# Performance work log

Hardware: AMD Instinct MI355X
Metric: run time of the kernel (lower is better)

The kernel has to match this reference:

```python
import jax, jax.numpy as jnp
import numpy as np

EMB = 300
NUM_LAYERS = 5
ATOM_DIMS = [119, 4, 12, 12, 10, 6, 6, 2, 2]
BOND_DIMS = [5, 6, 2]
BN_EPS = 1e-5


def setup_inputs() -> dict:
    key = jax.random.key(0)
    ks = jax.random.split(key, 16)
    N, E = 100000, 200000
    x_feat = jax.random.randint(ks[0], (N, 9), 0, 2, dtype=jnp.int32)
    edge_index = jax.random.randint(ks[1], (2, E), 0, N, dtype=jnp.int32)
    edge_attr = jax.random.randint(ks[2], (E, 3), 0, 2, dtype=jnp.int32)
    # atom embedding tables padded to max atom dim 119: [9, 119, EMB]
    atom_emb = jax.random.normal(ks[3], (9, max(ATOM_DIMS), EMB), jnp.float32) * 0.1
    # per-layer bond tables padded to max bond dim 6: [L, 3, 6, EMB]
    bond_emb = jax.random.normal(ks[4], (NUM_LAYERS, 3, max(BOND_DIMS), EMB), jnp.float32) * 0.1
    eps = jnp.zeros((NUM_LAYERS,), jnp.float32)  # GIN eps init 0
    s1 = 1.0 / np.sqrt(EMB)
    s2 = 1.0 / np.sqrt(2 * EMB)
    W1 = jax.random.uniform(ks[5], (NUM_LAYERS, EMB, 2 * EMB), jnp.float32, -s1, s1)
    b1 = jax.random.uniform(ks[6], (NUM_LAYERS, 2 * EMB), jnp.float32, -s1, s1)
    g1 = jnp.ones((NUM_LAYERS, 2 * EMB), jnp.float32)   # MLP BN gamma
    be1 = jnp.zeros((NUM_LAYERS, 2 * EMB), jnp.float32)  # MLP BN beta
    W2 = jax.random.uniform(ks[7], (NUM_LAYERS, 2 * EMB, EMB), jnp.float32, -s2, s2)
    b2 = jax.random.uniform(ks[8], (NUM_LAYERS, EMB), jnp.float32, -s2, s2)
    g2 = jnp.ones((NUM_LAYERS, EMB), jnp.float32)    # outer BN gamma
    be2 = jnp.zeros((NUM_LAYERS, EMB), jnp.float32)  # outer BN beta
    return dict(x_feat=x_feat, edge_index=edge_index, edge_attr=edge_attr,
                atom_emb=atom_emb, bond_emb=bond_emb, eps=eps,
                W1=W1, b1=b1, g1=g1, be1=be1, W2=W2, b2=b2, g2=g2, be2=be2)


def _batchnorm(h, gamma, beta):
    mu = h.mean(axis=0)
    var = h.var(axis=0)  # biased, as torch BN uses for normalization
    return (h - mu) * jax.lax.rsqrt(var + BN_EPS) * gamma + beta


def reference(x_feat, edge_index, edge_attr, atom_emb, bond_emb, eps,
              W1, b1, g1, be1, W2, b2, g2, be2):
    N = x_feat.shape[0]
    src, dst = edge_index[0], edge_index[1]  # x_j = x[src], aggregate at dst
    # atom encoder: sum of 9 embedding lookups -> [N, EMB]
    h = atom_emb[jnp.arange(9), x_feat].sum(axis=1)
    for l in range(NUM_LAYERS):
        # bond encoder: sum of 3 embedding lookups -> [E, EMB]
        e = bond_emb[l][jnp.arange(3), edge_attr].sum(axis=1)
        # message: relu(x_j + edge_emb); aggregate: scatter-add over dst
        msg = jax.nn.relu(h[src] + e)
        agg = jax.ops.segment_sum(msg, dst, num_segments=N)
        z = (1.0 + eps[l]) * h + agg
        # MLP: Linear -> BN -> ReLU -> Linear
        z = jnp.einsum('nd,df->nf', z, W1[l]) + b1[l]
        z = jax.nn.relu(_batchnorm(z, g1[l], be1[l]))
        z = jnp.einsum('nf,fd->nd', z, W2[l]) + b2[l]
        # outer BatchNorm, then ReLU except on last layer (dropout p=0 is no-op)
        z = _batchnorm(z, g2[l], be2[l])
        h = z if l == NUM_LAYERS - 1 else jax.nn.relu(z)
    return h  # JK='last'
```

## Files before the change

### kernel.cpp

```cpp
#include <hip/hip_runtime.h>

#define NL    5
#define NN    100000
#define NE    200000
#define MPAD  100096
#define MTILES 782
#define K1    320
#define N1    640
#define K2    640
#define N2    384
#define BN_EPS 1e-5f
#define G1    (MTILES * 5)
#define G2    (MTILES * 3)
#define NB_SCAN 98

typedef __attribute__((ext_vector_type(8))) short   short8;
typedef __attribute__((ext_vector_type(4))) float   floatx4;

__device__ inline void splitbf(float x, unsigned short& hi, unsigned short& lo) {
    unsigned u = __float_as_uint(x);
    unsigned hb = u & 0xFFFF0000u;
    float lf = x - __uint_as_float(hb);
    hi = (unsigned short)(u >> 16);
    lo = (unsigned short)(__float_as_uint(lf) >> 16);
}
__device__ inline unsigned short f2bf(float f) {
    unsigned u = __float_as_uint(f);
    unsigned r = u + 0x7FFFu + ((u >> 16) & 1u);
    return (unsigned short)(r >> 16);
}
__device__ inline float bf2f(unsigned short b) {
    return __uint_as_float(((unsigned)b) << 16);
}

__device__ inline void swz(int id, int G, int NC, int& row, int& col) {
    int q = G >> 3, r = G & 7;
    int x = id & 7, k = id >> 3;
    int w = x * q + (x < r ? x : r) + k;
    row = w / NC; col = w % NC;
}

__global__ void prep_w1(const float* __restrict__ W1,
                        unsigned short* __restrict__ Whi, unsigned short* __restrict__ Wlo) {
    int idx = blockIdx.x * blockDim.x + threadIdx.x;
    if (idx >= NL * N1 * K1) return;
    int l = idx / (N1 * K1);
    int rem = idx % (N1 * K1);
    int n = rem / K1;
    int k = rem % K1;
    float v = (k < 300 && n < 600) ? W1[((long)l * 300 + k) * 600 + n] : 0.f;
    unsigned short hi, lo; splitbf(v, hi, lo);
    Whi[idx] = hi; Wlo[idx] = lo;
}

__global__ void prep_w2(const float* __restrict__ W2,
                        unsigned short* __restrict__ Whi, unsigned short* __restrict__ Wlo) {
    int idx = blockIdx.x * blockDim.x + threadIdx.x;
    if (idx >= NL * N2 * K2) return;
    int l = idx / (N2 * K2);
    int rem = idx % (N2 * K2);
    int d = rem / K2;
    int k = rem % K2;
    float v = (d < 300 && k < 600) ? W2[((long)l * 600 + k) * 300 + d] : 0.f;
    unsigned short hi, lo; splitbf(v, hi, lo);
    Whi[idx] = hi; Wlo[idx] = lo;
}

__global__ void prep_vec(const float* __restrict__ b1, const float* __restrict__ g1, const float* __restrict__ be1,
                         const float* __restrict__ b2, const float* __restrict__ g2, const float* __restrict__ be2,
                         float* __restrict__ b1p, float* __restrict__ g1p, float* __restrict__ be1p,
                         float* __restrict__ b2p, float* __restrict__ g2p, float* __restrict__ be2p) {
    int idx = blockIdx.x * blockDim.x + threadIdx.x;
    if (idx < NL * N1) {
        int l = idx / N1, n = idx % N1;
        bool ok = (n < 600);
        b1p[idx]  = ok ? b1[l * 600 + n]  : 0.f;
        g1p[idx]  = ok ? g1[l * 600 + n]  : 0.f;
        be1p[idx] = ok ? be1[l * 600 + n] : 0.f;
    }
    if (idx < NL * N2) {
        int l = idx / N2, d = idx % N2;
        bool ok = (d < 300);
        b2p[idx]  = ok ? b2[l * 300 + d]  : 0.f;
        g2p[idx]  = ok ? g2[l * 300 + d]  : 0.f;
        be2p[idx] = ok ? be2[l * 300 + d] : 0.f;
    }
}

__global__ void atom_enc(const int* __restrict__ xf, const float* __restrict__ tab,
                         float* __restrict__ h) {
    int idx = blockIdx.x * blockDim.x + threadIdx.x;
    if (idx >= NN * 75) return;
    int n = idx / 75;
    int c = (idx % 75) * 4;
    float4 s = make_float4(0.f, 0.f, 0.f, 0.f);
#pragma unroll
    for (int f = 0; f < 9; f++) {
        int v = xf[n * 9 + f];
        const float4 t = *(const float4*)(tab + (long)(f * 119 + v) * 300 + c);
        s.x += t.x; s.y += t.y; s.z += t.z; s.w += t.w;
    }
    *(float4*)(h + (long)n * 300 + c) = s;
}

__global__ void count_deg(const int* __restrict__ ei, int* __restrict__ deg) {
    int e = blockIdx.x * blockDim.x + threadIdx.x;
    if (e >= NE) return;
    atomicAdd(&deg[ei[NE + e]], 1);
}

__global__ void block_deg_sum(const int* __restrict__ deg, int* __restrict__ bsum) {
    __shared__ int tmp[1024];
    const int t = threadIdx.x;
    const int idx = blockIdx.x * 1024 + t;
    tmp[t] = (idx < NN) ? deg[idx] : 0;
    __syncthreads();
    for (int o = 512; o > 0; o >>= 1) {
        if (t < o) tmp[t] += tmp[t + o];
        __syncthreads();
    }
    if (t == 0) bsum[blockIdx.x] = tmp[0];
}

__global__ void scan_rowptr2(const int* __restrict__ deg, const int* __restrict__ bsum,
                             int* __restrict__ rowptr) {
    __shared__ int tmp[1024];
    __shared__ int sbase;
    const int b = blockIdx.x;
    const int t = threadIdx.x;
    tmp[t] = (t < b) ? bsum[t] : 0;
    __syncthreads();
    for (int o = 512; o > 0; o >>= 1) {
        if (t < o) tmp[t] += tmp[t + o];
        __syncthreads();
    }
    if (t == 0) sbase = tmp[0];
    __syncthreads();
    const int base = sbase;
    const int idx = b * 1024 + t;
    const int d = (idx < NN) ? deg[idx] : 0;
    tmp[t] = d;
    __syncthreads();
    for (int o = 1; o < 1024; o <<= 1) {
        int u = (t >= o) ? tmp[t - o] : 0;
        __syncthreads();
        tmp[t] += u;
        __syncthreads();
    }
    if (idx < NN) rowptr[idx] = base + tmp[t] - d;
    if (idx == NN - 1) rowptr[NN] = base + tmp[t];
}

__global__ void fill_csr(const int* __restrict__ ei, const int* __restrict__ ea,
                         const int* __restrict__ rowptr, int* __restrict__ fillc,
                         int* __restrict__ csr_src, int* __restrict__ csr_att) {
    int e = blockIdx.x * blockDim.x + threadIdx.x;
    if (e >= NE) return;
    int dst = ei[NE + e];
    int pos = atomicAdd(&fillc[dst], 1);
    int slot = rowptr[dst] + pos;
    csr_src[slot] = ei[e];
    csr_att[slot] = ea[e * 3] | (ea[e * 3 + 1] << 3) | (ea[e * 3 + 2] << 6);
}

__global__ void gather_zin(const float* __restrict__ hsrc,
                           const float* __restrict__ sc2v, const float* __restrict__ sh2v,
                           int use_bn,
                           const int* __restrict__ rowptr,
                           const int* __restrict__ csr_src, const int* __restrict__ csr_att,
                           const float* __restrict__ bond,
                           const float* __restrict__ eps, int l,
                           unsigned short* __restrict__ zin) {
    int idx = blockIdx.x * blockDim.x + threadIdx.x;
    if (idx >= NN * 80) return;
    int n = idx / 80;
    int c = (idx % 80) * 4;
    ushort4 hi4, lo4;
    if (c < 300) {
        float4 sc = make_float4(1.f, 1.f, 1.f, 1.f);
        float4 sh = make_float4(0.f, 0.f, 0.f, 0.f);
        if (use_bn) {
            sc = *(const float4*)(sc2v + c);
            sh = *(const float4*)(sh2v + c);
        }
        int p0 = rowptr[n], p1 = rowptr[n + 1];
        float4 s = make_float4(0.f, 0.f, 0.f, 0.f);
        for (int j = p0; j < p1; j++) {
            int src = csr_src[j];
            int att = csr_att[j];
            float4 hv = *(const float4*)(hsrc + (long)src * 300 + c);
            if (use_bn) {
                hv.x = fmaxf(hv.x * sc.x + sh.x, 0.f);
                hv.y = fmaxf(hv.y * sc.y + sh.y, 0.f);
                hv.z = fmaxf(hv.z * sc.z + sh.z, 0.f);
                hv.w = fmaxf(hv.w * sc.w + sh.w, 0.f);
            }
            const float4 t0 = *(const float4*)(bond + (0 * 6 + (att & 7)) * 300 + c);
            const float4 t1 = *(const float4*)(bond + (1 * 6 + ((att >> 3) & 7)) * 300 + c);
            const float4 t2 = *(const float4*)(bond + (2 * 6 + ((att >> 6) & 1)) * 300 + c);
            float m;
            m = hv.x + t0.x + t1.x + t2.x; s.x += (m > 0.f ? m : 0.f);
            m = hv.y + t0.y + t1.y + t2.y; s.y += (m > 0.f ? m : 0.f);
            m = hv.z + t0.z + t1.z + t2.z; s.z += (m > 0.f ? m : 0.f);
            m = hv.w + t0.w + t1.w + t2.w; s.w += (m > 0.f ? m : 0.f);
        }
        const float ep = 1.f + eps[l];
        float4 hn = *(const float4*)(hsrc + (long)n * 300 + c);
        if (use_bn) {
            hn.x = fmaxf(hn.x * sc.x + sh.x, 0.f);
            hn.y = fmaxf(hn.y * sc.y + sh.y, 0.f);
            hn.z = fmaxf(hn.z * sc.z + sh.z, 0.f);
            hn.w = fmaxf(hn.w * sc.w + sh.w, 0.f);
        }
        splitbf(ep * hn.x + s.x, hi4.x, lo4.x);
        splitbf(ep * hn.y + s.y, hi4.y, lo4.y);
        splitbf(ep * hn.z + s.z, hi4.z, lo4.z);
        splitbf(ep * hn.w + s.w, hi4.w, lo4.w);
    } else {
        hi4.x = hi4.y = hi4.z = hi4.w = 0;
        lo4.x = lo4.y = lo4.z = lo4.w = 0;
    }
    *(ushort4*)(zin + (long)n * 640 + c)       = hi4;
    *(ushort4*)(zin + (long)n * 640 + 320 + c) = lo4;
}


__global__ __launch_bounds__(256, 4)
void gemm1_pre(const unsigned short* __restrict__ zin,
               const unsigned short* __restrict__ Whi, const unsigned short* __restrict__ Wlo,
               const float* __restrict__ bias, unsigned short* __restrict__ z1b,
               float* __restrict__ stat_sum, float* __restrict__ stat_sq) {
    __shared__ unsigned short Ah[128 * 32], Al[128 * 32];
    __shared__ unsigned short Bh[128 * 32], Bl[128 * 32];
    __shared__ float ssum[128], ssq[128];

    const int tid  = threadIdx.x;
    const int wave = tid >> 6;
    const int lane = tid & 63;
    int rowb, colb; swz(blockIdx.x, G1, 5, rowb, colb);
    const long row0 = (long)rowb * 128;
    const long col0 = (long)colb * 128;

    floatx4 acc[4][4];
#pragma unroll
    for (int mi = 0; mi < 4; mi++)
#pragma unroll
        for (int ni = 0; ni < 4; ni++)
            acc[mi][ni] = (floatx4){0.f, 0.f, 0.f, 0.f};

    const int sr  = lane >> 2;
    const int scb = (((lane & 3) ^ ((sr >> 1) & 3))) * 8;
    const int wm  = (wave >> 1) * 64;
    const int wn  = (wave & 1) * 64;
    const int fr  = lane & 15;
    const int q   = lane >> 4;
    const int qs  = (q ^ ((fr >> 1) & 3)) * 8;

    for (int k0 = 0; k0 < K1; k0 += 32) {
#pragma unroll
        for (int i = 0; i < 2; i++) {
            int r = wave * 32 + i * 16;
            const unsigned short* gah = zin + (row0 + r + sr) * 640 + k0 + scb;
            const unsigned short* gbh = Whi + (col0 + r + sr) * (long)K1 + k0 + scb;
            const unsigned short* gbl = Wlo + (col0 + r + sr) * (long)K1 + k0 + scb;
            __builtin_amdgcn_global_load_lds((const __attribute__((address_space(1))) void*)gah,
                                             (__attribute__((address_space(3))) void*)(Ah + r * 32), 16, 0, 0);
            __builtin_amdgcn_global_load_lds((const __attribute__((address_space(1))) void*)(gah + 320),
                                             (__attribute__((address_space(3))) void*)(Al + r * 32), 16, 0, 0);
            __builtin_amdgcn_global_load_lds((const __attribute__((address_space(1))) void*)gbh,
                                             (__attribute__((address_space(3))) void*)(Bh + r * 32), 16, 0, 0);
            __builtin_amdgcn_global_load_lds((const __attribute__((address_space(1))) void*)gbl,
                                             (__attribute__((address_space(3))) void*)(Bl + r * 32), 16, 0, 0);
        }
        __syncthreads();
        short8 ah[4], alo[4], bh[4], blo[4];
#pragma unroll
        for (int mi = 0; mi < 4; mi++) {
            ah[mi]  = *(const short8*)(Ah + (wm + mi * 16 + fr) * 32 + qs);
            alo[mi] = *(const short8*)(Al + (wm + mi * 16 + fr) * 32 + qs);
        }
#pragma unroll
        for (int ni = 0; ni < 4; ni++) {
            bh[ni]  = *(const short8*)(Bh + (wn + ni * 16 + fr) * 32 + qs);
            blo[ni] = *(const short8*)(Bl + (wn + ni * 16 + fr) * 32 + qs);
        }
#pragma unroll
        for (int mi = 0; mi < 4; mi++)
#pragma unroll
            for (int ni = 0; ni < 4; ni++) {
                acc[mi][ni] = __builtin_amdgcn_mfma_f32_16x16x32_bf16(ah[mi],  bh[ni],  acc[mi][ni], 0, 0, 0);
                acc[mi][ni] = __builtin_amdgcn_mfma_f32_16x16x32_bf16(alo[mi], bh[ni],  acc[mi][ni], 0, 0, 0);
                acc[mi][ni] = __builtin_amdgcn_mfma_f32_16x16x32_bf16(ah[mi],  blo[ni], acc[mi][ni], 0, 0, 0);
            }
        __syncthreads();
    }

    if (tid < 128) { ssum[tid] = 0.f; ssq[tid] = 0.f; }
    __syncthreads();
#pragma unroll
    for (int ni = 0; ni < 4; ni++) {
        int cl = wn + ni * 16 + fr;
        long cg = col0 + cl;
        float bs = bias[cg];
        float psum = 0.f, psq = 0.f;
#pragma unroll
        for (int mi = 0; mi < 4; mi++) {
#pragma unroll
            for (int r = 0; r < 4; r++) {
                long rg = row0 + wm + mi * 16 + q * 4 + r;
                float v = acc[mi][ni][r] + bs;
                z1b[rg * N1 + cg] = f2bf(v);
                if (rg < NN) { psum += v; psq += v * v; }
            }
        }
        atomicAdd(&ssum[cl], psum);
        atomicAdd(&ssq[cl], psq);
    }
    __syncthreads();
    if (tid < 128) {
        atomicAdd(&stat_sum[col0 + tid], ssum[tid]);
        atomicAdd(&stat_sq[col0 + tid], ssq[tid]);
    }
}

__global__ __launch_bounds__(256, 4)
void gemm2_fused(const unsigned short* __restrict__ z1b,
                 const float* __restrict__ scale, const float* __restrict__ shift,
                 const unsigned short* __restrict__ Whi, const unsigned short* __restrict__ Wlo,
                 const float* __restrict__ bias, float* __restrict__ z2f,
                 float* __restrict__ stat_sum, float* __restrict__ stat_sq) {
    __shared__ unsigned short Ah[128 * 32], Al[128 * 32];
    __shared__ unsigned short Bh[128 * 32], Bl[128 * 32];
    __shared__ float sSc[K2], sSh[K2];
    __shared__ float ssum[128], ssq[128];

    const int tid  = threadIdx.x;
    const int wave = tid >> 6;
    const int lane = tid & 63;
    int rowb, colb; swz(blockIdx.x, G2, 3, rowb, colb);
    const long row0 = (long)rowb * 128;
    const long col0 = (long)colb * 128;

    for (int i = tid; i < K2; i += 256) { sSc[i] = scale[i]; sSh[i] = shift[i]; }

    floatx4 acc[4][4];
#pragma unroll
    for (int mi = 0; mi < 4; mi++)
#pragma unroll
        for (int ni = 0; ni < 4; ni++)
            acc[mi][ni] = (floatx4){0.f, 0.f, 0.f, 0.f};

    const int sr  = lane >> 2;
    const int scb = (((lane & 3) ^ ((sr >> 1) & 3))) * 8;
    const int wm  = (wave >> 1) * 64;
    const int wn  = (wave & 1) * 64;
    const int fr  = lane & 15;
    const int q   = lane >> 4;
    const int qs  = (q ^ ((fr >> 1) & 3)) * 8;
    const int arow = tid >> 1;
    const int acb  = (tid & 1) * 16;
    const int akey = (arow >> 1) & 3;
    const long grow = row0 + arow;
    __syncthreads();

    for (int k0 = 0; k0 < K2; k0 += 32) {
#pragma unroll
        for (int i = 0; i < 2; i++) {
            int r = wave * 32 + i * 16;
            const unsigned short* gbh = Whi + (col0 + r + sr) * (long)K2 + k0 + scb;
            const unsigned short* gbl = Wlo + (col0 + r + sr) * (long)K2 + k0 + scb;
            __builtin_amdgcn_global_load_lds((const __attribute__((address_space(1))) void*)gbh,
                                             (__attribute__((address_space(3))) void*)(Bh + r * 32), 16, 0, 0);
            __builtin_amdgcn_global_load_lds((const __attribute__((address_space(1))) void*)gbl,
                                             (__attribute__((address_space(3))) void*)(Bl + r * 32), 16, 0, 0);
        }
#pragma unroll
        for (int j = 0; j < 4; j++) {
            int cc = k0 + acb + j * 4;
            ushort4 xv = *(const ushort4*)(z1b + grow * K2 + cc);
            const float4 sc = *(const float4*)(sSc + cc);
            const float4 sh = *(const float4*)(sSh + cc);
            ushort4 hi4, lo4;
            splitbf(fmaxf(bf2f(xv.x) * sc.x + sh.x, 0.f), hi4.x, lo4.x);
            splitbf(fmaxf(bf2f(xv.y) * sc.y + sh.y, 0.f), hi4.y, lo4.y);
            splitbf(fmaxf(bf2f(xv.z) * sc.z + sh.z, 0.f), hi4.z, lo4.z);
            splitbf(fmaxf(bf2f(xv.w) * sc.w + sh.w, 0.f), hi4.w, lo4.w);
            int slog = (acb >> 3) + (j >> 1);
            int pcol = ((slog ^ akey) << 3) + (j & 1) * 4;
            *(ushort4*)(Ah + arow * 32 + pcol) = hi4;
            *(ushort4*)(Al + arow * 32 + pcol) = lo4;
        }
        __syncthreads();
        short8 ah[4], alo[4], bh[4], blo[4];
#pragma unroll
        for (int mi = 0; mi < 4; mi++) {
            ah[mi]  = *(const short8*)(Ah + (wm + mi * 16 + fr) * 32 + qs);
            alo[mi] = *(const short8*)(Al + (wm + mi * 16 + fr) * 32 + qs);
        }
#pragma unroll
        for (int ni = 0; ni < 4; ni++) {
            bh[ni]  = *(const short8*)(Bh + (wn + ni * 16 + fr) * 32 + qs);
            blo[ni] = *(const short8*)(Bl + (wn + ni * 16 + fr) * 32 + qs);
        }
#pragma unroll
        for (int mi = 0; mi < 4; mi++)
#pragma unroll
            for (int ni = 0; ni < 4; ni++) {
                acc[mi][ni] = __builtin_amdgcn_mfma_f32_16x16x32_bf16(ah[mi],  bh[ni],  acc[mi][ni], 0, 0, 0);
                acc[mi][ni] = __builtin_amdgcn_mfma_f32_16x16x32_bf16(alo[mi], bh[ni],  acc[mi][ni], 0, 0, 0);
                acc[mi][ni] = __builtin_amdgcn_mfma_f32_16x16x32_bf16(ah[mi],  blo[ni], acc[mi][ni], 0, 0, 0);
            }
        __syncthreads();
    }

    if (tid < 128) { ssum[tid] = 0.f; ssq[tid] = 0.f; }
    __syncthreads();
#pragma unroll
    for (int ni = 0; ni < 4; ni++) {
        int cl = wn + ni * 16 + fr;
        long cg = col0 + cl;
        float bs = bias[cg];
        float psum = 0.f, psq = 0.f;
#pragma unroll
        for (int mi = 0; mi < 4; mi++) {
#pragma unroll
            for (int r = 0; r < 4; r++) {
                long rg = row0 + wm + mi * 16 + q * 4 + r;
                float v = acc[mi][ni][r] + bs;
                if (cg < 300) z2f[rg * 300 + cg] = v;
                if (rg < NN) { psum += v; psq += v * v; }
            }
        }
        atomicAdd(&ssum[cl], psum);
        atomicAdd(&ssq[cl], psq);
    }
    __syncthreads();
    if (tid < 128) {
        atomicAdd(&stat_sum[col0 + tid], ssum[tid]);
        atomicAdd(&stat_sq[col0 + tid], ssq[tid]);
    }
}

__global__ void bn_finalize(const float* __restrict__ sum, const float* __restrict__ sq,
                            const float* __restrict__ g, const float* __restrict__ be,
                            float* __restrict__ scale, float* __restrict__ shift, int n) {
    int c = blockIdx.x * blockDim.x + threadIdx.x;
    if (c >= n) return;
    const float invN = 1.f / (float)NN;
    float mu  = sum[c] * invN;
    float var = sq[c] * invN - mu * mu;
    float rs  = rsqrtf(var + BN_EPS);
    float s   = rs * g[c];
    scale[c] = s;
    shift[c] = be[c] - mu * s;
}

__global__ void bn2_out(const float* __restrict__ z2,
                        const float* __restrict__ scale, const float* __restrict__ shift,
                        float* __restrict__ out, int do_relu) {
    int idx = blockIdx.x * blockDim.x + threadIdx.x;
    if (idx >= NN * 75) return;
    int n = idx / 75;
    int c = (idx % 75) * 4;
    const float4 v  = *(const float4*)(z2 + (long)n * 300 + c);
    const float4 sc = *(const float4*)(scale + c);
    const float4 sh = *(const float4*)(shift + c);
    float4 o;
    o.x = v.x * sc.x + sh.x;
    o.y = v.y * sc.y + sh.y;
    o.z = v.z * sc.z + sh.z;
    o.w = v.w * sc.w + sh.w;
    if (do_relu) {
        o.x = fmaxf(o.x, 0.f); o.y = fmaxf(o.y, 0.f);
        o.z = fmaxf(o.z, 0.f); o.w = fmaxf(o.w, 0.f);
    }
    *(float4*)(out + (long)n * 300 + c) = o;
}

extern "C" void kernel_launch(void* const* d_in, const int* in_sizes, int n_in,
                              void* d_out, int out_size, void* d_ws, size_t ws_size,
                              hipStream_t stream) {
    const int*   xf   = (const int*)d_in[0];
    const int*   ei   = (const int*)d_in[1];
    const int*   ea   = (const int*)d_in[2];
    const float* atab = (const float*)d_in[3];
    const float* btab = (const float*)d_in[4];
    const float* eps  = (const float*)d_in[5];
    const float* W1   = (const float*)d_in[6];
    const float* b1   = (const float*)d_in[7];
    const float* g1   = (const float*)d_in[8];
    const float* be1  = (const float*)d_in[9];
    const float* W2   = (const float*)d_in[10];
    const float* b2   = (const float*)d_in[11];
    const float* g2   = (const float*)d_in[12];
    const float* be2  = (const float*)d_in[13];
    float* hbuf = (float*)d_out;

    char* ws = (char*)d_ws;
    size_t off = 0;
    auto alloc = [&](size_t bytes) { size_t o = off; off += (bytes + 255) & ~(size_t)255; return o; };
    char* R0c = ws + alloc((size_t)MPAD * 640 * 2);
    char* R1c = ws + alloc((size_t)MPAD * 640 * 2);
    unsigned short* W1hi = (unsigned short*)(ws + alloc((size_t)NL * N1 * K1 * 2));
    unsigned short* W1lo = (unsigned short*)(ws + alloc((size_t)NL * N1 * K1 * 2));
    unsigned short* W2hi = (unsigned short*)(ws + alloc((size_t)NL * N2 * K2 * 2));
    unsigned short* W2lo = (unsigned short*)(ws + alloc((size_t)NL * N2 * K2 * 2));
    float* b1p  = (float*)(ws + alloc((size_t)NL * N1 * 4));
    float* g1p  = (float*)(ws + alloc((size_t)NL * N1 * 4));
    float* be1p = (float*)(ws + alloc((size_t)NL * N1 * 4));
    float* b2p  = (float*)(ws + alloc((size_t)NL * N2 * 4));
    float* g2p  = (float*)(ws + alloc((size_t)NL * N2 * 4));
    float* be2p = (float*)(ws + alloc((size_t)NL * N2 * 4));
    float* sums = (float*)(ws + alloc(2048 * 4));
    float* scale1 = (float*)(ws + alloc(N1 * 4));
    float* shift1 = (float*)(ws + alloc(N1 * 4));
    float* scale2 = (float*)(ws + alloc(N2 * 4));
    float* shift2 = (float*)(ws + alloc(N2 * 4));
    int* deg     = (int*)(ws + alloc((size_t)NN * 4));
    int* fillc   = (int*)(ws + alloc((size_t)NN * 4));
    int* rowptr  = (int*)(ws + alloc((size_t)(NN + 1) * 4));
    int* csr_src = (int*)(ws + alloc((size_t)NE * 4));
    int* csr_att = (int*)(ws + alloc((size_t)NE * 4));
    int* bsum    = (int*)(ws + alloc((size_t)NB_SCAN * 4));
    (void)ws_size; (void)in_sizes; (void)n_in; (void)out_size;

    prep_w1<<<(NL * N1 * K1 + 255) / 256, 256, 0, stream>>>(W1, W1hi, W1lo);
    prep_w2<<<(NL * N2 * K2 + 255) / 256, 256, 0, stream>>>(W2, W2hi, W2lo);
    prep_vec<<<(NL * N1 + 255) / 256, 256, 0, stream>>>(b1, g1, be1, b2, g2, be2,
                                                        b1p, g1p, be1p, b2p, g2p, be2p);
    atom_enc<<<(NN * 75 + 255) / 256, 256, 0, stream>>>(xf, atab, hbuf);
    hipMemsetAsync(deg, 0, (size_t)NN * 4, stream);
    hipMemsetAsync(fillc, 0, (size_t)NN * 4, stream);
    count_deg<<<(NE + 255) / 256, 256, 0, stream>>>(ei, deg);
    block_deg_sum<<<NB_SCAN, 1024, 0, stream>>>(deg, bsum);
    scan_rowptr2<<<NB_SCAN, 1024, 0, stream>>>(deg, bsum, rowptr);
    fill_csr<<<(NE + 255) / 256, 256, 0, stream>>>(ei, ea, rowptr, fillc, csr_src, csr_att);

    for (int l = 0; l < NL; l++) {
        char* Ra = (l & 1) ? R1c : R0c;
        char* Rb = (l & 1) ? R0c : R1c;
        unsigned short* zin = (unsigned short*)Ra;
        unsigned short* z1b = (unsigned short*)Rb;
        float*          z2f = (float*)Ra;
        const float*    z2p = (const float*)Rb;

        hipMemsetAsync(sums, 0, 2048 * 4, stream);
        gather_zin<<<(NN * 80 + 255) / 256, 256, 0, stream>>>(
            (l == 0) ? hbuf : z2p, scale2, shift2, (l == 0) ? 0 : 1,
            rowptr, csr_src, csr_att, btab + (size_t)l * 5400, eps, l, zin);
        gemm1_pre<<<G1, 256, 0, stream>>>(
            zin, W1hi + (size_t)l * N1 * K1, W1lo + (size_t)l * N1 * K1,
            b1p + l * N1, z1b, sums + 0, sums + 640);
        bn_finalize<<<(N1 + 255) / 256, 256, 0, stream>>>(sums + 0, sums + 640,
            g1p + l * N1, be1p + l * N1, scale1, shift1, N1);
        gemm2_fused<<<G2, 256, 0, stream>>>(
            z1b, scale1, shift1, W2hi + (size_t)l * N2 * K2, W2lo + (size_t)l * N2 * K2,
            b2p + l * N2, z2f, sums + 1280, sums + 1664);
        bn_finalize<<<(N2 + 255) / 256, 256, 0, stream>>>(sums + 1280, sums + 1664,
            g2p + l * N2, be2p + l * N2, scale2, shift2, N2);
    }
    bn2_out<<<(NN * 75 + 255) / 256, 256, 0, stream>>>(
        (const float*)R0c, scale2, shift2, hbuf, 0);
}
```

Baseline: 2.295 ms.

## Enlarge GEMM block tiles to 256x128 with 128x64 per-wave tiles

Both MLP GEMM kernels now compute a 256-row by 128-column output tile per block instead of 128x128. Each wave owns a 128x64 sub-tile with 32 accumulators, and the A fragments are loaded per mi inside the MFMA loop. The goal is to halve the number of row tiles and reuse each B tile across twice as many rows, cutting global and LDS traffic per MFMA. The cost is more registers and LDS per block, so occupancy drops to 2 blocks per SIMD-launch bound. MPAD (100096) divides evenly by 256, giving 391 row tiles.

```diff
diff --git a/kernel.cpp b/kernel.cpp
--- a/kernel.cpp
+++ b/kernel.cpp
@@ -4,14 +4,14 @@
 #define NN    100000
 #define NE    200000
 #define MPAD  100096
-#define MTILES 782
+#define MT2   391
 #define K1    320
 #define N1    640
 #define K2    640
 #define N2    384
 #define BN_EPS 1e-5f
-#define G1    (MTILES * 5)
-#define G2    (MTILES * 3)
+#define G1    (MT2 * 5)
+#define G2    (MT2 * 3)
 #define NB_SCAN 98
 
 typedef __attribute__((ext_vector_type(8))) short   short8;
@@ -225,12 +225,12 @@
 }
 
 
-__global__ __launch_bounds__(256, 4)
+__global__ __launch_bounds__(256, 2)
 void gemm1_pre(const unsigned short* __restrict__ zin,
                const unsigned short* __restrict__ Whi, const unsigned short* __restrict__ Wlo,
                const float* __restrict__ bias, unsigned short* __restrict__ z1b,
                float* __restrict__ stat_sum, float* __restrict__ stat_sq) {
-    __shared__ unsigned short Ah[128 * 32], Al[128 * 32];
+    __shared__ unsigned short Ah[256 * 32], Al[256 * 32];
     __shared__ unsigned short Bh[128 * 32], Bl[128 * 32];
     __shared__ float ssum[128], ssq[128];
 
@@ -238,60 +238,62 @@
     const int wave = tid >> 6;
     const int lane = tid & 63;
     int rowb, colb; swz(blockIdx.x, G1, 5, rowb, colb);
-    const long row0 = (long)rowb * 128;
+    const long row0 = (long)rowb * 256;
     const long col0 = (long)colb * 128;
 
-    floatx4 acc[4][4];
-#pragma unroll
-    for (int mi = 0; mi < 4; mi++)
+    floatx4 acc[8][4];
+#pragma unroll
+    for (int mi = 0; mi < 8; mi++)
 #pragma unroll
         for (int ni = 0; ni < 4; ni++)
             acc[mi][ni] = (floatx4){0.f, 0.f, 0.f, 0.f};
 
     const int sr  = lane >> 2;
     const int scb = (((lane & 3) ^ ((sr >> 1) & 3))) * 8;
-    const int wm  = (wave >> 1) * 64;
-    const int wn  = (wave & 1) * 64;
+    const int wm2 = (wave >> 1) * 128;
+    const int wn2 = (wave & 1) * 64;
     const int fr  = lane & 15;
     const int q   = lane >> 4;
     const int qs  = (q ^ ((fr >> 1) & 3)) * 8;
 
     for (int k0 = 0; k0 < K1; k0 += 32) {
 #pragma unroll
-        for (int i = 0; i < 2; i++) {
-            int r = wave * 32 + i * 16;
+        for (int i = 0; i < 4; i++) {
+            int r = wave * 64 + i * 16;
             const unsigned short* gah = zin + (row0 + r + sr) * 640 + k0 + scb;
-            const unsigned short* gbh = Whi + (col0 + r + sr) * (long)K1 + k0 + scb;
-            const unsigned short* gbl = Wlo + (col0 + r + sr) * (long)K1 + k0 + scb;
             __builtin_amdgcn_global_load_lds((const __attribute__((address_space(1))) void*)gah,
                                              (__attribute__((address_space(3))) void*)(Ah + r * 32), 16, 0, 0);
             __builtin_amdgcn_global_load_lds((const __attribute__((address_space(1))) void*)(gah + 320),
                                              (__attribute__((address_space(3))) void*)(Al + r * 32), 16, 0, 0);
+        }
+#pragma unroll
+        for (int i = 0; i < 2; i++) {
+            int r = wave * 32 + i * 16;
+            const unsigned short* gbh = Whi + (col0 + r + sr) * (long)K1 + k0 + scb;
+            const unsigned short* gbl = Wlo + (col0 + r + sr) * (long)K1 + k0 + scb;
             __builtin_amdgcn_global_load_lds((const __attribute__((address_space(1))) void*)gbh,
                                              (__attribute__((address_space(3))) void*)(Bh + r * 32), 16, 0, 0);
             __builtin_amdgcn_global_load_lds((const __attribute__((address_space(1))) void*)gbl,
                                              (__attribute__((address_space(3))) void*)(Bl + r * 32), 16, 0, 0);
         }
         __syncthreads();
-        short8 ah[4], alo[4], bh[4], blo[4];
-#pragma unroll
-        for (int mi = 0; mi < 4; mi++) {
-            ah[mi]  = *(const short8*)(Ah + (wm + mi * 16 + fr) * 32 + qs);
-            alo[mi] = *(const short8*)(Al + (wm + mi * 16 + fr) * 32 + qs);
-        }
+        short8 bh[4], blo[4];
 #pragma unroll
         for (int ni = 0; ni < 4; ni++) {
-            bh[ni]  = *(const short8*)(Bh + (wn + ni * 16 + fr) * 32 + qs);
-            blo[ni] = *(const short8*)(Bl + (wn + ni * 16 + fr) * 32 + qs);
-        }
-#pragma unroll
-        for (int mi = 0; mi < 4; mi++)
+            bh[ni]  = *(const short8*)(Bh + (wn2 + ni * 16 + fr) * 32 + qs);
+            blo[ni] = *(const short8*)(Bl + (wn2 + ni * 16 + fr) * 32 + qs);
+        }
+#pragma unroll
+        for (int mi = 0; mi < 8; mi++) {
+            short8 ah  = *(const short8*)(Ah + (wm2 + mi * 16 + fr) * 32 + qs);
+            short8 alo = *(const short8*)(Al + (wm2 + mi * 16 + fr) * 32 + qs);
 #pragma unroll
             for (int ni = 0; ni < 4; ni++) {
-                acc[mi][ni] = __builtin_amdgcn_mfma_f32_16x16x32_bf16(ah[mi],  bh[ni],  acc[mi][ni], 0, 0, 0);
-                acc[mi][ni] = __builtin_amdgcn_mfma_f32_16x16x32_bf16(alo[mi], bh[ni],  acc[mi][ni], 0, 0, 0);
-                acc[mi][ni] = __builtin_amdgcn_mfma_f32_16x16x32_bf16(ah[mi],  blo[ni], acc[mi][ni], 0, 0, 0);
+                acc[mi][ni] = __builtin_amdgcn_mfma_f32_16x16x32_bf16(ah,  bh[ni],  acc[mi][ni], 0, 0, 0);
+                acc[mi][ni] = __builtin_amdgcn_mfma_f32_16x16x32_bf16(alo, bh[ni],  acc[mi][ni], 0, 0, 0);
+                acc[mi][ni] = __builtin_amdgcn_mfma_f32_16x16x32_bf16(ah,  blo[ni], acc[mi][ni], 0, 0, 0);
             }
+        }
         __syncthreads();
     }
 
@@ -299,15 +301,15 @@
     __syncthreads();
 #pragma unroll
     for (int ni = 0; ni < 4; ni++) {
-        int cl = wn + ni * 16 + fr;
+        int cl = wn2 + ni * 16 + fr;
         long cg = col0 + cl;
         float bs = bias[cg];
         float psum = 0.f, psq = 0.f;
 #pragma unroll
-        for (int mi = 0; mi < 4; mi++) {
+        for (int mi = 0; mi < 8; mi++) {
 #pragma unroll
             for (int r = 0; r < 4; r++) {
-                long rg = row0 + wm + mi * 16 + q * 4 + r;
+                long rg = row0 + wm2 + mi * 16 + q * 4 + r;
                 float v = acc[mi][ni][r] + bs;
                 z1b[rg * N1 + cg] = f2bf(v);
                 if (rg < NN) { psum += v; psq += v * v; }
@@ -323,13 +325,13 @@
     }
 }
 
-__global__ __launch_bounds__(256, 4)
+__global__ __launch_bounds__(256, 2)
 void gemm2_fused(const unsigned short* __restrict__ z1b,
                  const float* __restrict__ scale, const float* __restrict__ shift,
                  const unsigned short* __restrict__ Whi, const unsigned short* __restrict__ Wlo,
                  const float* __restrict__ bias, float* __restrict__ z2f,
                  float* __restrict__ stat_sum, float* __restrict__ stat_sq) {
-    __shared__ unsigned short Ah[128 * 32], Al[128 * 32];
+    __shared__ unsigned short Ah[256 * 32], Al[256 * 32];
     __shared__ unsigned short Bh[128 * 32], Bl[128 * 32];
     __shared__ float sSc[K2], sSh[K2];
     __shared__ float ssum[128], ssq[128];
@@ -338,29 +340,26 @@
     const int wave = tid >> 6;
     const int lane = tid & 63;
     int rowb, colb; swz(blockIdx.x, G2, 3, rowb, colb);
-    const long row0 = (long)rowb * 128;
+    const long row0 = (long)rowb * 256;
     const long col0 = (long)colb * 128;
 
     for (int i = tid; i < K2; i += 256) { sSc[i] = scale[i]; sSh[i] = shift[i]; }
 
-    floatx4 acc[4][4];
-#pragma unroll
-    for (int mi = 0; mi < 4; mi++)
+    floatx4 acc[8][4];
+#pragma unroll
+    for (int mi = 0; mi < 8; mi++)
 #pragma unroll
         for (int ni = 0; ni < 4; ni++)
             acc[mi][ni] = (floatx4){0.f, 0.f, 0.f, 0.f};
 
     const int sr  = lane >> 2;
     const int scb = (((lane & 3) ^ ((sr >> 1) & 3))) * 8;
-    const int wm  = (wave >> 1) * 64;
-    const int wn  = (wave & 1) * 64;
+    const int wm2 = (wave >> 1) * 128;
+    const int wn2 = (wave & 1) * 64;
     const int fr  = lane & 15;
     const int q   = lane >> 4;
     const int qs  = (q ^ ((fr >> 1) & 3)) * 8;
-    const int arow = tid >> 1;
-    const int acb  = (tid & 1) * 16;
-    const int akey = (arow >> 1) & 3;
-    const long grow = row0 + arow;
+    const int acb = (tid & 1) * 16;
     __syncthreads();
 
     for (int k0 = 0; k0 < K2; k0 += 32) {
@@ -375,41 +374,45 @@
                                              (__attribute__((address_space(3))) void*)(Bl + r * 32), 16, 0, 0);
         }
 #pragma unroll
-        for (int j = 0; j < 4; j++) {
-            int cc = k0 + acb + j * 4;
-            ushort4 xv = *(const ushort4*)(z1b + grow * K2 + cc);
-            const float4 sc = *(const float4*)(sSc + cc);
-            const float4 sh = *(const float4*)(sSh + cc);
-            ushort4 hi4, lo4;
-            splitbf(fmaxf(bf2f(xv.x) * sc.x + sh.x, 0.f), hi4.x, lo4.x);
-            splitbf(fmaxf(bf2f(xv.y) * sc.y + sh.y, 0.f), hi4.y, lo4.y);
-            splitbf(fmaxf(bf2f(xv.z) * sc.z + sh.z, 0.f), hi4.z, lo4.z);
-            splitbf(fmaxf(bf2f(xv.w) * sc.w + sh.w, 0.f), hi4.w, lo4.w);
-            int slog = (acb >> 3) + (j >> 1);
-            int pcol = ((slog ^ akey) << 3) + (j & 1) * 4;
-            *(ushort4*)(Ah + arow * 32 + pcol) = hi4;
-            *(ushort4*)(Al + arow * 32 + pcol) = lo4;
-        }
-        __syncthreads();
-        short8 ah[4], alo[4], bh[4], blo[4];
-#pragma unroll
-        for (int mi = 0; mi < 4; mi++) {
-            ah[mi]  = *(const short8*)(Ah + (wm + mi * 16 + fr) * 32 + qs);
-            alo[mi] = *(const short8*)(Al + (wm + mi * 16 + fr) * 32 + qs);
-        }
+        for (int h = 0; h < 2; h++) {
+            int ar = (tid >> 1) + h * 128;
+            long gr = row0 + ar;
+            int akey = (ar >> 1) & 3;
+#pragma unroll
+            for (int j = 0; j < 4; j++) {
+                int cc = k0 + acb + j * 4;
+                ushort4 xv = *(const ushort4*)(z1b + gr * K2 + cc);
+                const float4 sc = *(const float4*)(sSc + cc);
+                const float4 sh = *(const float4*)(sSh + cc);
+                ushort4 hi4, lo4;
+                splitbf(fmaxf(bf2f(xv.x) * sc.x + sh.x, 0.f), hi4.x, lo4.x);
+                splitbf(fmaxf(bf2f(xv.y) * sc.y + sh.y, 0.f), hi4.y, lo4.y);
+                splitbf(fmaxf(bf2f(xv.z) * sc.z + sh.z, 0.f), hi4.z, lo4.z);
+                splitbf(fmaxf(bf2f(xv.w) * sc.w + sh.w, 0.f), hi4.w, lo4.w);
+                int slog = (acb >> 3) + (j >> 1);
+                int pcol = ((slog ^ akey) << 3) + (j & 1) * 4;
+                *(ushort4*)(Ah + ar * 32 + pcol) = hi4;
+                *(ushort4*)(Al + ar * 32 + pcol) = lo4;
+            }
+        }
+        __syncthreads();
+        short8 bh[4], blo[4];
 #pragma unroll
         for (int ni = 0; ni < 4; ni++) {
-            bh[ni]  = *(const short8*)(Bh + (wn + ni * 16 + fr) * 32 + qs);
-            blo[ni] = *(const short8*)(Bl + (wn + ni * 16 + fr) * 32 + qs);
-        }
-#pragma unroll
-        for (int mi = 0; mi < 4; mi++)
+            bh[ni]  = *(const short8*)(Bh + (wn2 + ni * 16 + fr) * 32 + qs);
+            blo[ni] = *(const short8*)(Bl + (wn2 + ni * 16 + fr) * 32 + qs);
+        }
+#pragma unroll
+        for (int mi = 0; mi < 8; mi++) {
+            short8 ah  = *(const short8*)(Ah + (wm2 + mi * 16 + fr) * 32 + qs);
+            short8 alo = *(const short8*)(Al + (wm2 + mi * 16 + fr) * 32 + qs);
 #pragma unroll
             for (int ni = 0; ni < 4; ni++) {
-                acc[mi][ni] = __builtin_amdgcn_mfma_f32_16x16x32_bf16(ah[mi],  bh[ni],  acc[mi][ni], 0, 0, 0);
-                acc[mi][ni] = __builtin_amdgcn_mfma_f32_16x16x32_bf16(alo[mi], bh[ni],  acc[mi][ni], 0, 0, 0);
-                acc[mi][ni] = __builtin_amdgcn_mfma_f32_16x16x32_bf16(ah[mi],  blo[ni], acc[mi][ni], 0, 0, 0);
+                acc[mi][ni] = __builtin_amdgcn_mfma_f32_16x16x32_bf16(ah,  bh[ni],  acc[mi][ni], 0, 0, 0);
+                acc[mi][ni] = __builtin_amdgcn_mfma_f32_16x16x32_bf16(alo, bh[ni],  acc[mi][ni], 0, 0, 0);
+                acc[mi][ni] = __builtin_amdgcn_mfma_f32_16x16x32_bf16(ah,  blo[ni], acc[mi][ni], 0, 0, 0);
             }
+        }
         __syncthreads();
     }
 
@@ -417,15 +420,15 @@
     __syncthreads();
 #pragma unroll
     for (int ni = 0; ni < 4; ni++) {
-        int cl = wn + ni * 16 + fr;
+        int cl = wn2 + ni * 16 + fr;
         long cg = col0 + cl;
         float bs = bias[cg];
         float psum = 0.f, psq = 0.f;
 #pragma unroll
-        for (int mi = 0; mi < 4; mi++) {
+        for (int mi = 0; mi < 8; mi++) {
 #pragma unroll
             for (int r = 0; r < 4; r++) {
-                long rg = row0 + wm + mi * 16 + q * 4 + r;
+                long rg = row0 + wm2 + mi * 16 + q * 4 + r;
                 float v = acc[mi][ni][r] + bs;
                 if (cg < 300) z2f[rg * 300 + cg] = v;
                 if (rg < NN) { psum += v; psq += v * v; }
```

Result: no change. 2.300 ms (+0.2%).
